# Optimization experiments

Measured on AMD Instinct MI355X. Metric: run time of the kernel, lower is better.

## Reference

```python
import jax, jax.numpy as jnp
import numpy as np

WS = 16            # window size (patch grid)
NP = WS * WS       # 256 patch tokens
N = NP + 1         # +1 CLS
H = 16             # heads
LN_EPS = 1e-5


def _rel_pos_index():
    ch, cw = np.meshgrid(np.arange(WS), np.arange(WS), indexing='ij')
    flat = np.stack([ch.reshape(-1), cw.reshape(-1)])            # [2, NP]
    rel = flat[:, :, None] - flat[:, None, :]                    # [2, NP, NP]
    rel = rel.transpose(1, 2, 0).astype(np.int64)                # [NP, NP, 2]
    rel[:, :, 0] += WS - 1
    rel[:, :, 1] += WS - 1
    rel[:, :, 0] *= 2 * WS - 1
    nrd = (2 * WS - 1) * (2 * WS - 1) + 3                        # 964
    idx = np.zeros((N, N), dtype=np.int64)
    idx[1:, 1:] = rel.sum(-1)
    idx[0, 0:] = nrd - 3
    idx[0:, 0] = nrd - 2
    idx[0, 0] = nrd - 1
    return idx

REL_IDX = _rel_pos_index()


def layernorm(x, g, b):
    mu = x.mean(-1, keepdims=True)
    var = x.var(-1, keepdims=True)
    return (x - mu) * jax.lax.rsqrt(var + LN_EPS) * g + b


def rotate_half(t):
    t1, t2 = t[..., ::2], t[..., 1::2]
    return jnp.stack([-t2, t1], axis=-1).reshape(t.shape)


def apply_rope(t, cos, sin):
    # t: [B, H, NP, hd]; cos/sin: [NP, hd]
    return t * cos + rotate_half(t) * sin


def setup_inputs() -> dict:
    key = jax.random.key(0)
    ks = jax.random.split(key, 20)
    D, Hd = 1024, 4096
    s = lambda d: 1.0 / np.sqrt(d)
    return {
        'x': jax.random.normal(ks[0], (64, N, D), jnp.float32),
        'rope_cos': jnp.cos(jnp.arange(NP)[:, None] * jnp.exp(-jnp.arange(64) / 16.0)[None, :]),
        'rope_sin': jnp.sin(jnp.arange(NP)[:, None] * jnp.exp(-jnp.arange(64) / 16.0)[None, :]),
        'q_w': jax.random.normal(ks[1], (D, D)) * s(D),
        'q_b': jnp.zeros((D,)),
        'k_w': jax.random.normal(ks[2], (D, D)) * s(D),
        'v_w': jax.random.normal(ks[3], (D, D)) * s(D),
        'v_b': jnp.zeros((D,)),
        'rel_bias_table': jax.random.normal(ks[4], (964, H)) * 0.02,
        'inner_ln_g': jnp.ones((D,)), 'inner_ln_b': jnp.zeros((D,)),
        'proj_w': jax.random.normal(ks[5], (D, D)) * s(D),
        'proj_b': jnp.zeros((D,)),
        'norm1_g': jnp.ones((D,)), 'norm1_b': jnp.zeros((D,)),
        'norm2_g': jnp.ones((D,)), 'norm2_b': jnp.zeros((D,)),
        'w1_w': jax.random.normal(ks[6], (Hd, D)) * s(D),
        'w1_b': jnp.zeros((Hd,)),
        'w2_w': jax.random.normal(ks[7], (Hd, D)) * s(D),
        'w2_b': jnp.zeros((Hd,)),
        'ffn_ln_g': jnp.ones((Hd,)), 'ffn_ln_b': jnp.zeros((Hd,)),
        'w3_w': jax.random.normal(ks[8], (D, Hd)) * s(Hd),
        'w3_b': jnp.zeros((D,)),
    }


def reference(x, rope_cos, rope_sin, q_w, q_b, k_w, v_w, v_b, rel_bias_table,
              inner_ln_g, inner_ln_b, proj_w, proj_b, norm1_g, norm1_b,
              norm2_g, norm2_b, w1_w, w1_b, w2_w, w2_b, ffn_ln_g, ffn_ln_b,
              w3_w, w3_b):
    B, Ntok, D = x.shape
    hd = D // H
    scale = hd ** -0.5

    # ---- attention branch (pre-norm, subln path) ----
    xn = layernorm(x, norm1_g, norm1_b)
    q = (xn @ q_w.T + q_b).reshape(B, Ntok, H, hd).transpose(0, 2, 1, 3)
    k = (xn @ k_w.T).reshape(B, Ntok, H, hd).transpose(0, 2, 1, 3)
    v = (xn @ v_w.T + v_b).reshape(B, Ntok, H, hd).transpose(0, 2, 1, 3)

    # RoPE on all tokens except CLS
    q = jnp.concatenate([q[:, :, :1], apply_rope(q[:, :, 1:], rope_cos, rope_sin)], axis=2)
    k = jnp.concatenate([k[:, :, :1], apply_rope(k[:, :, 1:], rope_cos, rope_sin)], axis=2)

    attn = jnp.einsum('bhqd,bhkd->bhqk', q * scale, k)
    # relative position bias: [N, N, H] -> [H, N, N]
    rel_bias = rel_bias_table[REL_IDX.reshape(-1)].reshape(Ntok, Ntok, H).transpose(2, 0, 1)
    attn = attn + rel_bias[None]
    attn = jax.nn.softmax(attn, axis=-1)

    out = jnp.einsum('bhqk,bhkd->bqhd', attn, v).reshape(B, Ntok, D)
    out = layernorm(out, inner_ln_g, inner_ln_b)     # inner_attn_ln (subln)
    out = out @ proj_w.T + proj_b
    x = x + out

    # ---- SwiGLU MLP branch ----
    xn2 = layernorm(x, norm2_g, norm2_b)
    x1 = xn2 @ w1_w.T + w1_b
    x2 = xn2 @ w2_w.T + w2_b
    hidden = jax.nn.silu(x1) * x2
    hidden = layernorm(hidden, ffn_ln_g, ffn_ln_b)   # ffn_ln (subln)
    x = x + (hidden @ w3_w.T + w3_b)
    return x
```

## Files before the change

kernel.cpp:

```cpp
#include <hip/hip_runtime.h>
#include <stdint.h>

typedef __bf16 bf16;
typedef __attribute__((ext_vector_type(8))) __bf16 bf16x8;
typedef __attribute__((ext_vector_type(4))) float floatx4;

__device__ inline float bflo(uint32_t u){ union{uint32_t v; float f;} t; t.v = u << 16; return t.f; }
__device__ inline float bfhi(uint32_t u){ union{uint32_t v; float f;} t; t.v = u & 0xffff0000u; return t.f; }
__device__ inline uint32_t pack2(float a, float b){ union{ bf16 h[2]; uint32_t u; } t; t.h[0]=(bf16)a; t.h[1]=(bf16)b; return t.u; }

__device__ inline void load4(const bf16* p, float* x){
  uint2 u = *(const uint2*)p; x[0]=bflo(u.x); x[1]=bfhi(u.x); x[2]=bflo(u.y); x[3]=bfhi(u.y);
}
__device__ inline void load4(const float* p, float* x){
  float4 u = *(const float4*)p; x[0]=u.x; x[1]=u.y; x[2]=u.z; x[3]=u.w;
}

__device__ inline void gload16(const void* g, void* l){
  __builtin_amdgcn_global_load_lds((const __attribute__((address_space(1))) uint32_t*)g,
                                   (__attribute__((address_space(3))) uint32_t*)l, 16, 0, 0);
}

__global__ __launch_bounds__(256) void cvt_kernel(const float* __restrict__ in, bf16* __restrict__ out,
                                                  int n8, float scale)
{
  int i = blockIdx.x * 256 + threadIdx.x;
  if (i >= n8) return;
  const float* p = in + (size_t)i * 8;
  float4 a = *(const float4*)p;
  float4 b = *(const float4*)(p + 4);
  union{ uint4 q; bf16 h[8]; } pk;
  pk.h[0]=(bf16)(a.x*scale); pk.h[1]=(bf16)(a.y*scale); pk.h[2]=(bf16)(a.z*scale); pk.h[3]=(bf16)(a.w*scale);
  pk.h[4]=(bf16)(b.x*scale); pk.h[5]=(bf16)(b.y*scale); pk.h[6]=(bf16)(b.z*scale); pk.h[7]=(bf16)(b.w*scale);
  *(uint4*)(out + (size_t)i*8) = pk.q;
}

__global__ __launch_bounds__(256) void qkvb_fill(const float* __restrict__ qb, const float* __restrict__ vb,
                                                 float* __restrict__ out)
{
  int i = blockIdx.x * 256 + threadIdx.x;
  float v = 0.f;
  if (i < 1024) v = qb[i] * 0.125f;
  else if (i >= 2048) v = vb[i - 2048];
  out[i] = v;
}

__global__ __launch_bounds__(256) void bias_fill(const float* __restrict__ tab, bf16* __restrict__ biasB)
{
  int t = blockIdx.x * 256 + threadIdx.x;
  if (t >= 16*272*272) return;
  int kg = t % 272;
  int rem = t / 272;
  int qg = rem % 272;
  int h = rem / 272;
  float v;
  if (kg > 256) v = -3e38f;
  else {
    int qq = min(qg, 256);
    int idx;
    if (qq == 0 && kg == 0) idx = 963;
    else if (qq == 0) idx = 961;
    else if (kg == 0) idx = 962;
    else { int p = qq - 1, pk = kg - 1;
           idx = ((p >> 4) - (pk >> 4) + 15) * 31 + ((p & 15) - (pk & 15) + 15); }
    v = tab[idx*16 + h];
  }
  biasB[t] = (bf16)v;
}

template<int W, typename TIN>
__global__ __launch_bounds__(256) void ln_kernel(const TIN* in, const float* __restrict__ g,
                                                 const float* __restrict__ bb, bf16* out, int M)
{
  constexpr int E = W / 256;
  int row = blockIdx.x; if (row >= M) return;
  int tid = threadIdx.x;
  const TIN* rp = in + (size_t)row * W + tid * E;
  float x[E];
  #pragma unroll
  for (int j = 0; j < E; j += 4) load4(rp + j, &x[j]);
  float s = 0.f, ss = 0.f;
  #pragma unroll
  for (int e = 0; e < E; e++){ s += x[e]; ss += x[e]*x[e]; }
  #pragma unroll
  for (int k = 32; k >= 1; k >>= 1){ s += __shfl_xor(s, k, 64); ss += __shfl_xor(ss, k, 64); }
  __shared__ float rs_[4], rq_[4];
  if ((tid & 63) == 0){ rs_[tid >> 6] = s; rq_[tid >> 6] = ss; }
  __syncthreads();
  s = rs_[0]+rs_[1]+rs_[2]+rs_[3]; ss = rq_[0]+rq_[1]+rq_[2]+rq_[3];
  float mean = s * (1.0f / W);
  float var  = ss * (1.0f / W) - mean * mean;
  float rinv = rsqrtf(var + 1e-5f);
  bf16* op = out + (size_t)row * W + tid * E;
  const float* gp = g + tid * E;
  const float* bp = bb + tid * E;
  #pragma unroll
  for (int j = 0; j < E; j += 4){
    float gv[4], bv[4];
    load4(gp + j, gv); load4(bp + j, bv);
    float y0 = (x[j]  -mean)*rinv*gv[0] + bv[0];
    float y1 = (x[j+1]-mean)*rinv*gv[1] + bv[1];
    float y2 = (x[j+2]-mean)*rinv*gv[2] + bv[2];
    float y3 = (x[j+3]-mean)*rinv*gv[3] + bv[3];
    uint2 o; o.x = pack2(y0, y1); o.y = pack2(y2, y3);
    *(uint2*)(op + j) = o;
  }
}

template<typename TE, typename TC>
__global__ __launch_bounds__(256) void gemm_bt(const bf16* __restrict__ A, const bf16* __restrict__ Bw,
                                               const float* __restrict__ bias, const TE* extra,
                                               TC* C, int M, int N, int K, int mode)
{
  __shared__ __align__(16) bf16 As[128*32];
  __shared__ __align__(16) bf16 Bs[128*32];
  int tid = threadIdx.x;
  int lane = tid & 63, wave = tid >> 6;
  int l16 = lane & 15, quad = lane >> 4;
  int wm = wave >> 1, wn = wave & 1;
  int m0 = blockIdx.y * 128, n0 = blockIdx.x * 128;
  floatx4 acc[4][4];
  #pragma unroll
  for (int i = 0; i < 4; i++)
    #pragma unroll
    for (int j = 0; j < 4; j++) acc[i][j] = (floatx4){0.f,0.f,0.f,0.f};
  int nk = K >> 5;
  int rowS = tid >> 2;
  int colS = (tid & 3) * 8;
  int ra0 = min(m0 + rowS,      M-1);
  int ra1 = min(m0 + 64 + rowS, M-1);
  int rb0 = min(n0 + rowS,      N-1);
  int rb1 = min(n0 + 64 + rowS, N-1);
  const bf16* pa0 = A  + (size_t)ra0 * K + colS;
  const bf16* pa1 = A  + (size_t)ra1 * K + colS;
  const bf16* pb0 = Bw + (size_t)rb0 * K + colS;
  const bf16* pb1 = Bw + (size_t)rb1 * K + colS;
  bf16* la0 = &As[tid*8];        bf16* la1 = &As[2048 + tid*8];
  bf16* lb0 = &Bs[tid*8];        bf16* lb1 = &Bs[2048 + tid*8];
  auto stage = [&](int kt){
    int ko = kt * 32;
    gload16(pa0 + ko, la0);
    gload16(pa1 + ko, la1);
    gload16(pb0 + ko, lb0);
    gload16(pb1 + ko, lb1);
  };
  stage(0);
  int kt = 0;
  while (true){
    __syncthreads();
    bf16x8 af[4], bfv[4];
    #pragma unroll
    for (int i = 0; i < 4; i++) af[i]  = *(const bf16x8*)&As[(wm*64 + i*16 + l16)*32 + quad*8];
    #pragma unroll
    for (int j = 0; j < 4; j++) bfv[j] = *(const bf16x8*)&Bs[(wn*64 + j*16 + l16)*32 + quad*8];
    ++kt;
    bool more = kt < nk;
    if (more){
      __syncthreads();
      stage(kt);
    }
    #pragma unroll
    for (int i = 0; i < 4; i++)
      #pragma unroll
      for (int j = 0; j < 4; j++)
        acc[i][j] = __builtin_amdgcn_mfma_f32_16x16x32_bf16(af[i], bfv[j], acc[i][j], 0, 0, 0);
    if (!more) break;
  }
  #pragma unroll
  for (int i = 0; i < 4; i++){
    int gmb = m0 + wm*64 + i*16 + quad*4;
    #pragma unroll
    for (int j = 0; j < 4; j++){
      int gn = n0 + wn*64 + j*16 + l16;
      float bv = bias ? bias[gn] : 0.f;
      #pragma unroll
      for (int r = 0; r < 4; r++){
        int gm = gmb + r;
        if (gm < M){
          float v = acc[i][j][r] + bv;
          if (mode == 1) v += (float)extra[(size_t)gm * N + gn];
          else if (mode == 2){ float a = (float)extra[(size_t)gm * N + gn]; v *= a / (1.f + __expf(-a)); }
          C[(size_t)gm * N + gn] = (TC)v;
        }
      }
    }
  }
}

__global__ __launch_bounds__(256) void rope_kernel(bf16* __restrict__ qkv,
                                                   const float* __restrict__ cs, const float* __restrict__ sn)
{
  uint32_t i = blockIdx.x * 256u + threadIdx.x;
  int d0 = (int)(i & 511) * 2;
  int tok = (int)((i >> 9) & 255);
  int b = (int)(i >> 17);
  int j = d0 & 63;
  float c0 = cs[tok*64 + j], c1 = cs[tok*64 + j + 1];
  float s0 = sn[tok*64 + j], s1 = sn[tok*64 + j + 1];
  size_t off = ((size_t)(b*257 + tok + 1)) * 3072 + d0;
  uint32_t uq = *(const uint32_t*)(qkv + off);
  float x0 = bflo(uq), x1 = bfhi(uq);
  *(uint32_t*)(qkv + off) = pack2(x0*c0 - x1*s0, x1*c1 + x0*s1);
  uint32_t uk = *(const uint32_t*)(qkv + off + 1024);
  float y0 = bflo(uk), y1 = bfhi(uk);
  *(uint32_t*)(qkv + off + 1024) = pack2(y0*c0 - y1*s0, y1*c1 + y0*s1);
}

__global__ __launch_bounds__(256, 2) void attn_kernel(const bf16* __restrict__ QKV,
                                                      const bf16* __restrict__ biasB,
                                                      bf16* __restrict__ AO)
{
  constexpr int VS = 280;
  __shared__ __align__(16) bf16 Ks[272*64];
  __shared__ __align__(16) bf16 Vt[64*VS];
  __shared__ __align__(16) bf16 Os[4][16*72];
  int id = blockIdx.x;
  int h = id & 15, b = id >> 4;
  int tid = threadIdx.x, lane = tid & 63, wave = tid >> 6;
  int l16 = lane & 15, quad = lane >> 4;
  size_t baseQ = (size_t)(b*257) * 3072 + h*64;
  const bf16* Kg = QKV + baseQ + 1024;
  const bf16* Vg = QKV + baseQ + 2048;
  size_t aoBase = (size_t)(b*257) * 1024 + h*64;

  for (int i = tid; i < 272*8; i += 256){
    int row = i >> 3, seg = i & 7;
    int tok = min(row, 256);
    gload16(Kg + (size_t)tok*3072 + ((seg ^ (row & 7)) * 8), &Ks[i*8]);
  }
  for (int i = tid; i < 272*8; i += 256){
    int row = i >> 3, seg = i & 7;
    int tok = min(row, 256);
    uint4 v = *(const uint4*)(Vg + (size_t)tok*3072 + seg*8);
    uint4 w;
    w.x = (uint32_t)__shfl_xor((int)v.x, 8, 64);
    w.y = (uint32_t)__shfl_xor((int)v.y, 8, 64);
    w.z = (uint32_t)__shfl_xor((int)v.z, 8, 64);
    w.w = (uint32_t)__shfl_xor((int)v.w, 8, 64);
    union { uint4 q4; bf16 h8[8]; } mv, pv; mv.q4 = v; pv.q4 = w;
    int rb = row & ~1;
    if ((row & 1) == 0){
      #pragma unroll
      for (int jj = 0; jj < 4; jj++){
        union { uint32_t u; bf16 hh[2]; } pk; pk.hh[0] = mv.h8[jj]; pk.hh[1] = pv.h8[jj];
        *(uint32_t*)&Vt[(seg*8 + jj)*VS + rb] = pk.u;
      }
    } else {
      #pragma unroll
      for (int jj = 4; jj < 8; jj++){
        union { uint32_t u; bf16 hh[2]; } pk; pk.hh[0] = pv.h8[jj]; pk.hh[1] = mv.h8[jj];
        *(uint32_t*)&Vt[(seg*8 + jj)*VS + rb] = pk.u;
      }
    }
  }
  __syncthreads();

  int srcA = l16 + 16*((2*quad)     & 3);
  int srcB = l16 + 16*((2*quad + 1) & 3);

  for (int qt = wave; qt < 17; qt += 4){
    int q0 = qt * 16;
    int qrow = min(q0 + l16, 256);
    const bf16* qp = QKV + baseQ + (size_t)qrow*3072;
    bf16x8 qb0 = *(const bf16x8*)(qp + quad*8);
    bf16x8 qb1 = *(const bf16x8*)(qp + 32 + quad*8);

    const bf16* bp = biasB + ((size_t)(h*272) + (q0 + l16)) * 272;
    uint2 bu[17];
    #pragma unroll
    for (int nt = 0; nt < 17; nt++) bu[nt] = *(const uint2*)(bp + nt*16 + quad*4);

    floatx4 S[17];
    #pragma unroll
    for (int nt = 0; nt < 17; nt++){
      int row = nt*16 + l16;
      bf16x8 ka0 = *(const bf16x8*)&Ks[row*64 + ((quad     ^ (l16 & 7)) * 8)];
      bf16x8 ka1 = *(const bf16x8*)&Ks[row*64 + (((4+quad) ^ (l16 & 7)) * 8)];
      floatx4 c = (floatx4){0.f,0.f,0.f,0.f};
      c = __builtin_amdgcn_mfma_f32_16x16x32_bf16(ka0, qb0, c, 0, 0, 0);
      c = __builtin_amdgcn_mfma_f32_16x16x32_bf16(ka1, qb1, c, 0, 0, 0);
      S[nt] = c;
    }

    float m = -3e38f;
    #pragma unroll
    for (int nt = 0; nt < 17; nt++){
      S[nt][0] += bflo(bu[nt].x); S[nt][1] += bfhi(bu[nt].x);
      S[nt][2] += bflo(bu[nt].y); S[nt][3] += bfhi(bu[nt].y);
      m = fmaxf(m, fmaxf(fmaxf(S[nt][0], S[nt][1]), fmaxf(S[nt][2], S[nt][3])));
    }
    m = fmaxf(m, __shfl_xor(m, 16, 64));
    m = fmaxf(m, __shfl_xor(m, 32, 64));

    float lsum = 0.f;
    uint32_t pklo[17], pkhi[17];
    #pragma unroll
    for (int nt = 0; nt < 17; nt++){
      float p0 = __expf(S[nt][0] - m), p1 = __expf(S[nt][1] - m);
      float p2 = __expf(S[nt][2] - m), p3 = __expf(S[nt][3] - m);
      lsum += (p0 + p1) + (p2 + p3);
      pklo[nt] = pack2(p0, p1); pkhi[nt] = pack2(p2, p3);
    }
    lsum += __shfl_xor(lsum, 16, 64);
    lsum += __shfl_xor(lsum, 32, 64);

    floatx4 o[4];
    #pragma unroll
    for (int dt = 0; dt < 4; dt++) o[dt] = (floatx4){0.f,0.f,0.f,0.f};
    #pragma unroll
    for (int ks = 0; ks < 9; ks++){
      uint32_t t0[4], t1[4];
      t0[0] = (uint32_t)__shfl((int)pklo[2*ks], srcA, 64);
      t0[1] = (uint32_t)__shfl((int)pkhi[2*ks], srcA, 64);
      t0[2] = (uint32_t)__shfl((int)pklo[2*ks], srcB, 64);
      t0[3] = (uint32_t)__shfl((int)pkhi[2*ks], srcB, 64);
      if (2*ks + 1 <= 16){
        t1[0] = (uint32_t)__shfl((int)pklo[2*ks+1], srcA, 64);
        t1[1] = (uint32_t)__shfl((int)pkhi[2*ks+1], srcA, 64);
        t1[2] = (uint32_t)__shfl((int)pklo[2*ks+1], srcB, 64);
        t1[3] = (uint32_t)__shfl((int)pkhi[2*ks+1], srcB, 64);
      } else {
        t1[0] = 0; t1[1] = 0; t1[2] = 0; t1[3] = 0;
      }
      union { uint32_t u[4]; bf16x8 v; } pa;
      bool lowhalf = (quad < 2);
      pa.u[0] = lowhalf ? t0[0] : t1[0];
      pa.u[1] = lowhalf ? t0[1] : t1[1];
      pa.u[2] = lowhalf ? t0[2] : t1[2];
      pa.u[3] = lowhalf ? t0[3] : t1[3];
      #pragma unroll
      for (int dt = 0; dt < 4; dt++){
        bf16x8 vb = *(const bf16x8*)&Vt[(dt*16 + l16)*VS + ks*32 + quad*8];
        o[dt] = __builtin_amdgcn_mfma_f32_16x16x32_bf16(pa.v, vb, o[dt], 0, 0, 0);
      }
    }

    #pragma unroll
    for (int r = 0; r < 4; r++){
      int qr = quad*4 + r;
      float ls = __shfl(lsum, qr, 64);
      float rinv = 1.0f / ls;
      #pragma unroll
      for (int dt = 0; dt < 4; dt++)
        Os[wave][qr*72 + dt*16 + l16] = (bf16)(o[dt][r] * rinv);
    }
    #pragma unroll
    for (int half = 0; half < 2; half++){
      int rowL = (lane >> 3) + half*8;
      int chunk = lane & 7;
      int q = q0 + rowL;
      uint4 ov = *(const uint4*)&Os[wave][rowL*72 + chunk*8];
      if (q <= 256) *(uint4*)&AO[aoBase + (size_t)q*1024 + chunk*8] = ov;
    }
  }
}

extern "C" void kernel_launch(void* const* d_in, const int* in_sizes, int n_in,
                              void* d_out, int out_size, void* d_ws, size_t ws_size,
                              hipStream_t stream)
{
  (void)in_sizes; (void)n_in; (void)out_size; (void)ws_size;
  const float* x    = (const float*)d_in[0];
  const float* rc   = (const float*)d_in[1];
  const float* rsn  = (const float*)d_in[2];
  const float* q_w  = (const float*)d_in[3];
  const float* q_b  = (const float*)d_in[4];
  const float* k_w  = (const float*)d_in[5];
  const float* v_w  = (const float*)d_in[6];
  const float* v_b  = (const float*)d_in[7];
  const float* tab  = (const float*)d_in[8];
  const float* ig   = (const float*)d_in[9];
  const float* ib   = (const float*)d_in[10];
  const float* pw   = (const float*)d_in[11];
  const float* pb   = (const float*)d_in[12];
  const float* n1g  = (const float*)d_in[13];
  const float* n1b  = (const float*)d_in[14];
  const float* n2g  = (const float*)d_in[15];
  const float* n2b  = (const float*)d_in[16];
  const float* w1w  = (const float*)d_in[17];
  const float* w1b  = (const float*)d_in[18];
  const float* w2w  = (const float*)d_in[19];
  const float* w2b  = (const float*)d_in[20];
  const float* fg   = (const float*)d_in[21];
  const float* fb   = (const float*)d_in[22];
  const float* w3w  = (const float*)d_in[23];
  const float* w3b  = (const float*)d_in[24];

  const int M = 64 * 257;
  const int D = 1024, HD = 4096;
  char* ws = (char*)d_ws;
  const size_t CHB = (size_t)M * D * 2;
  bf16* B0 = (bf16*)(ws);
  bf16* B1 = (bf16*)(ws + CHB);
  bf16* B2 = (bf16*)(ws + 2*CHB);
  bf16* B3 = (bf16*)(ws + 3*CHB);
  bf16* WQ = (bf16*)(ws + 4*CHB);
  bf16* WK = WQ + (size_t)D*D;
  bf16* WV = WK + (size_t)D*D;
  bf16* WP = WV + (size_t)D*D;
  bf16* W1 = WP + (size_t)D*D;
  bf16* W2 = W1 + (size_t)HD*D;
  bf16* W3 = W2 + (size_t)HD*D;
  float* QKVB = (float*)(W3 + (size_t)HD*D);
  bf16* XN  = B0;
  bf16* QKV = B1;
  bf16* AO  = B0;
  bf16* AOL = B1;
  bf16* X1  = B2;
  bf16* XN2 = B3;
  bf16* HS  = B0;
  bf16* biasB = (bf16*)d_out;
  float* OUT = (float*)d_out;

  dim3 blk(256);
  dim3 g1(D/128, (M + 127)/128);
  dim3 gqkv(3072/128, (M + 127)/128);

  const int n8_D = D*D/8;
  const int n8_H = HD*D/8;
  cvt_kernel<<<dim3(n8_D/256), blk, 0, stream>>>(q_w, WQ, n8_D, 0.125f);
  cvt_kernel<<<dim3(n8_D/256), blk, 0, stream>>>(k_w, WK, n8_D, 1.f);
  cvt_kernel<<<dim3(n8_D/256), blk, 0, stream>>>(v_w, WV, n8_D, 1.f);
  cvt_kernel<<<dim3(n8_D/256), blk, 0, stream>>>(pw,  WP, n8_D, 1.f);
  cvt_kernel<<<dim3(n8_H/256), blk, 0, stream>>>(w1w, W1, n8_H, 1.f);
  cvt_kernel<<<dim3(n8_H/256), blk, 0, stream>>>(w2w, W2, n8_H, 1.f);
  cvt_kernel<<<dim3(n8_H/256), blk, 0, stream>>>(w3w, W3, n8_H, 1.f);
  qkvb_fill<<<dim3(12), blk, 0, stream>>>(q_b, v_b, QKVB);
  bias_fill<<<dim3((16*272*272 + 255)/256), blk, 0, stream>>>(tab, biasB);

  ln_kernel<1024, float><<<dim3(M), blk, 0, stream>>>(x, n1g, n1b, XN, M);
  gemm_bt<bf16, bf16><<<gqkv, blk, 0, stream>>>(XN, WQ, QKVB, (const bf16*)nullptr, QKV, M, 3072, D, 0);
  rope_kernel<<<dim3(64*256*512/256), blk, 0, stream>>>(QKV, rc, rsn);
  attn_kernel<<<dim3(64*16), blk, 0, stream>>>(QKV, biasB, AO);
  ln_kernel<1024, bf16><<<dim3(M), blk, 0, stream>>>(AO, ig, ib, AOL, M);
  gemm_bt<float, bf16><<<g1, blk, 0, stream>>>(AOL, WP, pb, x, X1, M, D, D, 1);
  ln_kernel<1024, bf16><<<dim3(M), blk, 0, stream>>>(X1, n2g, n2b, XN2, M);

  const int MC = M / 2;
  dim3 g2(HD/128, (MC + 127)/128);
  dim3 g1c(D/128, (MC + 127)/128);
  for (int c = 0; c < 2; c++){
    const bf16* a2 = XN2 + (size_t)c * MC * D;
    const bf16* x1 = X1  + (size_t)c * MC * D;
    float*      oc = OUT + (size_t)c * MC * D;
    gemm_bt<bf16, bf16><<<g2, blk, 0, stream>>>(a2, W1, w1b, (const bf16*)nullptr, HS, MC, HD, D, 0);
    gemm_bt<bf16, bf16><<<g2, blk, 0, stream>>>(a2, W2, w2b, HS, HS, MC, HD, D, 2);
    ln_kernel<4096, bf16><<<dim3(MC), blk, 0, stream>>>(HS, fg, fb, HS, MC);
    gemm_bt<bf16, float><<<g1c, blk, 0, stream>>>(HS, W3, w3b, x1, oc, MC, D, HD, 1);
  }
}
```

Before: 1.617 ms.

## Add 256x256-tile 512-thread GEMM with XCD remap for QKV and MLP up-projections

```diff
diff --git a/kernel.cpp b/kernel.cpp
--- a/kernel.cpp
+++ b/kernel.cpp
@@ -187,6 +187,112 @@
   }
 }
 
+template<typename TE, typename TC>
+__global__ __launch_bounds__(512) void gemm256(const bf16* __restrict__ A, const bf16* __restrict__ Bw,
+                                               const float* __restrict__ bias, const TE* extra,
+                                               TC* C, int M, int N, int K, int mode)
+{
+  __shared__ __align__(16) bf16 lds[65536];
+  int tid = threadIdx.x;
+  int lane = tid & 63, wave = tid >> 6;
+  int l16 = lane & 15, quad = lane >> 4;
+  int wm = wave >> 2, wn = wave & 3;
+
+  int nwg = gridDim.x * gridDim.y;
+  int orig = blockIdx.y * gridDim.x + blockIdx.x;
+  int qq = nwg >> 3, rr = nwg & 7;
+  int xcd = orig & 7, idx = orig >> 3;
+  int wg = (xcd < rr ? xcd*(qq+1) : rr*(qq+1) + (xcd-rr)*qq) + idx;
+  int bx = wg % gridDim.x, by = wg / gridDim.x;
+  int m0 = by * 256, n0 = bx * 256;
+
+  floatx4 acc[8][4];
+  #pragma unroll
+  for (int i = 0; i < 8; i++)
+    #pragma unroll
+    for (int j = 0; j < 4; j++) acc[i][j] = (floatx4){0.f,0.f,0.f,0.f};
+  int nk = K >> 6;
+
+  int srow = tid >> 3, sseg = tid & 7;
+  int sA = ((sseg ^ (srow & 7)) << 3);
+  const bf16* pA[4]; const bf16* pB[4];
+  #pragma unroll
+  for (int jj = 0; jj < 4; jj++){
+    pA[jj] = A  + (size_t)min(m0 + jj*64 + srow, M-1) * K + sA;
+    pB[jj] = Bw + (size_t)min(n0 + jj*64 + srow, N-1) * K + sA;
+  }
+  auto stage = [&](int kt, int b){
+    int ko = kt * 64;
+    bf16* as = lds + (b ? 16384 : 0);
+    bf16* bs = lds + 32768 + (b ? 16384 : 0);
+    #pragma unroll
+    for (int jj = 0; jj < 4; jj++){
+      gload16(pA[jj] + ko, as + jj*4096 + tid*8);
+      gload16(pB[jj] + ko, bs + jj*4096 + tid*8);
+    }
+  };
+
+  stage(0, 0);
+  int cur = 0;
+  for (int kt = 0; kt < nk; ++kt){
+    bool more = (kt + 1) < nk;
+    if (more){
+      stage(kt + 1, cur ^ 1);
+      asm volatile("s_waitcnt vmcnt(8)" ::: "memory");
+    } else {
+      asm volatile("s_waitcnt vmcnt(0)" ::: "memory");
+    }
+    __builtin_amdgcn_s_barrier();
+    asm volatile("" ::: "memory");
+    bf16* as = lds + (cur ? 16384 : 0);
+    bf16* bs = lds + 32768 + (cur ? 16384 : 0);
+    #pragma unroll
+    for (int kk = 0; kk < 2; kk++){
+      bf16x8 af[8], bfv[4];
+      #pragma unroll
+      for (int i = 0; i < 8; i++){
+        int r = wm*128 + i*16 + l16;
+        af[i] = *(const bf16x8*)&as[r*64 + (((kk*4 + quad) ^ (l16 & 7)) << 3)];
+      }
+      #pragma unroll
+      for (int j = 0; j < 4; j++){
+        int c = wn*64 + j*16 + l16;
+        bfv[j] = *(const bf16x8*)&bs[c*64 + (((kk*4 + quad) ^ (l16 & 7)) << 3)];
+      }
+      __builtin_amdgcn_s_setprio(1);
+      #pragma unroll
+      for (int i = 0; i < 8; i++)
+        #pragma unroll
+        for (int j = 0; j < 4; j++)
+          acc[i][j] = __builtin_amdgcn_mfma_f32_16x16x32_bf16(af[i], bfv[j], acc[i][j], 0, 0, 0);
+      __builtin_amdgcn_s_setprio(0);
+    }
+    asm volatile("" ::: "memory");
+    __builtin_amdgcn_s_barrier();
+    cur ^= 1;
+  }
+
+  #pragma unroll
+  for (int i = 0; i < 8; i++){
+    int gmb = m0 + wm*128 + i*16 + quad*4;
+    #pragma unroll
+    for (int j = 0; j < 4; j++){
+      int gn = n0 + wn*64 + j*16 + l16;
+      float bv = bias ? bias[gn] : 0.f;
+      #pragma unroll
+      for (int r = 0; r < 4; r++){
+        int gm = gmb + r;
+        if (gm < M){
+          float v = acc[i][j][r] + bv;
+          if (mode == 1) v += (float)extra[(size_t)gm * N + gn];
+          else if (mode == 2){ float a = (float)extra[(size_t)gm * N + gn]; v *= a / (1.f + __expf(-a)); }
+          C[(size_t)gm * N + gn] = (TC)v;
+        }
+      }
+    }
+  }
+}
+
 __global__ __launch_bounds__(256) void rope_kernel(bf16* __restrict__ qkv,
                                                    const float* __restrict__ cs, const float* __restrict__ sn)
 {
@@ -412,9 +518,9 @@
   bf16* biasB = (bf16*)d_out;
   float* OUT = (float*)d_out;
 
-  dim3 blk(256);
+  dim3 blk(256), blk2(512);
   dim3 g1(D/128, (M + 127)/128);
-  dim3 gqkv(3072/128, (M + 127)/128);
+  dim3 gqkv(3072/256, (M + 255)/256);
 
   const int n8_D = D*D/8;
   const int n8_H = HD*D/8;
@@ -429,7 +535,7 @@
   bias_fill<<<dim3((16*272*272 + 255)/256), blk, 0, stream>>>(tab, biasB);
 
   ln_kernel<1024, float><<<dim3(M), blk, 0, stream>>>(x, n1g, n1b, XN, M);
-  gemm_bt<bf16, bf16><<<gqkv, blk, 0, stream>>>(XN, WQ, QKVB, (const bf16*)nullptr, QKV, M, 3072, D, 0);
+  gemm256<bf16, bf16><<<gqkv, blk2, 0, stream>>>(XN, WQ, QKVB, (const bf16*)nullptr, QKV, M, 3072, D, 0);
   rope_kernel<<<dim3(64*256*512/256), blk, 0, stream>>>(QKV, rc, rsn);
   attn_kernel<<<dim3(64*16), blk, 0, stream>>>(QKV, biasB, AO);
   ln_kernel<1024, bf16><<<dim3(M), blk, 0, stream>>>(AO, ig, ib, AOL, M);
@@ -437,14 +543,14 @@
   ln_kernel<1024, bf16><<<dim3(M), blk, 0, stream>>>(X1, n2g, n2b, XN2, M);
 
   const int MC = M / 2;
-  dim3 g2(HD/128, (MC + 127)/128);
+  dim3 g2(HD/256, (MC + 255)/256);
   dim3 g1c(D/128, (MC + 127)/128);
   for (int c = 0; c < 2; c++){
     const bf16* a2 = XN2 + (size_t)c * MC * D;
     const bf16* x1 = X1  + (size_t)c * MC * D;
     float*      oc = OUT + (size_t)c * MC * D;
-    gemm_bt<bf16, bf16><<<g2, blk, 0, stream>>>(a2, W1, w1b, (const bf16*)nullptr, HS, MC, HD, D, 0);
-    gemm_bt<bf16, bf16><<<g2, blk, 0, stream>>>(a2, W2, w2b, HS, HS, MC, HD, D, 2);
+    gemm256<bf16, bf16><<<g2, blk2, 0, stream>>>(a2, W1, w1b, (const bf16*)nullptr, HS, MC, HD, D, 0);
+    gemm256<bf16, bf16><<<g2, blk2, 0, stream>>>(a2, W2, w2b, HS, HS, MC, HD, D, 2);
     ln_kernel<4096, bf16><<<dim3(MC), blk, 0, stream>>>(HS, fg, fb, HS, MC);
     gemm_bt<bf16, float><<<g1c, blk, 0, stream>>>(HS, W3, w3b, x1, oc, MC, D, HD, 1);
   }
```

Measured after the change: 1.857 ms. 1.15x slower.
